# Kernel optimization log

Measured on AMD Instinct MI355X. Metric: run time of the kernel, lower is better.

The kernel has to match this reference:

```python
import jax, jax.numpy as jnp
import numpy as np

B = 4096          # number of instance groups (images)
C = 81            # num_classes + 1 (fixed by the 81x81 prior_rel buffer)
D_K = 64
MAX_N = 128       # max instances per group


def setup_inputs() -> dict:
    key = jax.random.key(0)
    rng = np.random.default_rng(0)
    ni = rng.integers(1, MAX_N + 1, size=B)
    ni[0] = MAX_N  # pin the max so padded length is deterministic
    num_instances = jnp.asarray(ni, dtype=jnp.int32)
    total = int(ni.sum())
    ks = jax.random.split(key, 10)
    s_in = 1.0 / np.sqrt(C)
    s_dk = 1.0 / np.sqrt(D_K)
    return {
        'x': jax.random.normal(ks[0], (total, C), jnp.float32),
        'num_instances': num_instances,
        'prior_rel': jax.random.normal(ks[1], (C, C), jnp.float32) * s_in,
        'wq': jax.random.normal(ks[2], (C, D_K), jnp.float32) * s_in,
        'bq': jnp.zeros((D_K,), jnp.float32),
        'wk': jax.random.normal(ks[3], (C, D_K), jnp.float32) * s_in,
        'bk': jnp.zeros((D_K,), jnp.float32),
        'wv': jax.random.normal(ks[4], (C, D_K), jnp.float32) * s_in,
        'bv': jnp.zeros((D_K,), jnp.float32),
        'wu': jax.random.normal(ks[5], (D_K, C), jnp.float32) * s_dk,
        'bu': jnp.zeros((C,), jnp.float32),
    }


def reference(x, num_instances, prior_rel, wq, bq, wk, bk, wv, bv, wu, bu):
    # num_instances is static ragged metadata (the torch code keeps it as a
    # Python list), so it is safe to pull concrete ints from it here.
    ni = np.asarray(num_instances)
    Bn = ni.shape[0]
    M = int(ni.max())
    total = x.shape[0]

    counts = jnp.asarray(ni, jnp.int32)                      # [B]
    offsets = jnp.concatenate([jnp.zeros((1,), jnp.int32),
                               jnp.cumsum(counts)[:-1]])      # [B]
    pos = jnp.arange(M, dtype=jnp.int32)                      # [M]
    mask = pos[None, :] < counts[:, None]                     # [B, M] valid slots
    idx = offsets[:, None] + pos[None, :]                     # [B, M] flat gather idx
    idx_safe = jnp.where(mask, idx, 0)

    # pad: split x into ragged groups, zero-pad each to length M
    padded = x[idx_safe] * mask[:, :, None].astype(x.dtype)   # [B, M, C]

    q = padded @ wq + bq                                      # [B, M, d_k]
    k = padded @ wk + bk                                      # [B, M, d_k]
    v = (padded @ prior_rel) @ wv + bv                        # [B, M, d_k]

    scores = jnp.einsum('bmd,bnd->bmn', q, k) / jnp.sqrt(
        jnp.asarray(D_K, x.dtype))                            # [B, M, M]
    # mask padded KEY columns (queries on padded rows are dropped at unpad)
    scores = jnp.where(mask[:, None, :], scores, -jnp.inf)
    probs = jax.nn.softmax(scores, axis=2)
    out = jnp.einsum('bmn,bnd->bmd', probs, v)                # [B, M, d_k]
    out = out @ wu + bu                                       # [B, M, C]

    # unpad: scatter valid rows back to their ragged flat positions
    tgt = jnp.where(mask, idx, total)                         # dump pad rows past end
    flat = jnp.zeros((total + 1, out.shape[-1]), out.dtype)
    flat = flat.at[tgt.reshape(-1)].set(out.reshape(-1, out.shape[-1]))
    return flat[:total]
```

## Files before the change

kernel.cpp:

```cpp
#include <hip/hip_runtime.h>


typedef __attribute__((ext_vector_type(8))) short short8;
typedef __attribute__((ext_vector_type(4))) float f32x4;
typedef __attribute__((ext_vector_type(4))) short short4v;

constexpr int C  = 81;
constexpr int DK = 64;
constexpr int CP = 96;

constexpr int QK_STRIDE = 72;
constexpr int VT_STRIDE = 136;
constexpr int P_STRIDE  = 136;
constexpr int QS_STRIDE = 72;
constexpr int O_STRIDE  = 72;
constexpr int OFF_K  = 0;
constexpr int OFF_VT = OFF_K + 128 * QK_STRIDE;
constexpr int OFF_P  = OFF_VT + 64 * VT_STRIDE;
constexpr int SMEM_TOT = OFF_P + 4 * 16 * P_STRIDE;

__device__ inline ushort f2b(float f) {
    uint u = __float_as_uint(f);
    uint r = (u + 0x7fffu + ((u >> 16) & 1u)) >> 16;
    return (ushort)r;
}

#define MFMA16(a, b, c) __builtin_amdgcn_mfma_f32_16x16x32_bf16((a), (b), (c), 0, 0, 0)

__global__ void scan_counts(const int* __restrict__ counts,
                            int* __restrict__ offsets, int n) {
    __shared__ int part[256];
    int tid = threadIdx.x;
    int per = (n + 255) >> 8;
    int base = tid * per;
    int s = 0;
    for (int i = 0; i < per; i++) {
        int idx = base + i;
        if (idx < n) s += counts[idx];
    }
    part[tid] = s;
    __syncthreads();
    for (int off = 1; off < 256; off <<= 1) {
        int v = (tid >= off) ? part[tid - off] : 0;
        __syncthreads();
        part[tid] += v;
        __syncthreads();
    }
    int run = (tid == 0) ? 0 : part[tid - 1];
    for (int i = 0; i < per; i++) {
        int idx = base + i;
        if (idx < n) { offsets[idx] = run; run += counts[idx]; }
    }
}

__global__ void prep_weights(const float* __restrict__ prior,
                             const float* __restrict__ wq, const float* __restrict__ wk,
                             const float* __restrict__ wv, const float* __restrict__ wu,
                             ushort* __restrict__ wqT, ushort* __restrict__ wkT,
                             ushort* __restrict__ wvT, ushort* __restrict__ wuT) {
    int idx = blockIdx.x * 256 + threadIdx.x;
    int sec = idx / (DK * CP);
    int i   = idx - sec * (DK * CP);
    if (sec == 0 || sec == 1) {
        int n = i / CP, k = i - (i / CP) * CP;
        const float* w = (sec == 0) ? wq : wk;
        ushort* dst    = (sec == 0) ? wqT : wkT;
        dst[n * CP + k] = (k < C) ? f2b(w[k * DK + n]) : (ushort)0;
    } else if (sec == 2) {
        int n = i / CP, k = i - (i / CP) * CP;
        float s = 0.f;
        if (k < C)
            for (int e = 0; e < C; e++) s = fmaf(prior[k * C + e], wv[e * DK + n], s);
        wvT[n * CP + k] = (k < C) ? f2b(s) : (ushort)0;
    } else {
        int n = i / DK, k = i - (i / DK) * DK;
        wuT[n * DK + k] = (n < C) ? f2b(wu[k * C + n]) : (ushort)0;
    }
}

__launch_bounds__(256, 3)
__global__ void ravnet_mfma(const float* __restrict__ x,
                            const int* __restrict__ counts,
                            const int* __restrict__ offsets,
                            const ushort* __restrict__ wqT, const ushort* __restrict__ wkT,
                            const ushort* __restrict__ wvT, const ushort* __restrict__ wuT,
                            const float* __restrict__ bq, const float* __restrict__ bk,
                            const float* __restrict__ bv, const float* __restrict__ bu,
                            float* __restrict__ out) {
    __shared__ __align__(16) ushort sm[SMEM_TOT];

    const int b    = blockIdx.x;
    const int N    = counts[b];
    const long off = offsets[b];
    const int tid  = threadIdx.x;
    const int lane = tid & 63;
    const int wave = tid >> 6;
    const int quad = lane >> 4;
    const int m16  = lane & 15;
    const int NT8  = (N + 15) >> 4;
    const int NT4  = (N + 31) >> 5;
    const float* xsrc = x + off * C;

    short4v qreg[2][4];

    #pragma unroll
    for (int t = 0; t < 2; t++) {
        const int rt = wave + 4 * t;
        if (rt < NT8) {
            const int row  = rt * 16 + m16;
            const bool vrow = row < N;
            const float* xr = xsrc + (long)(vrow ? row : (N - 1)) * C;
            short8 ax[3];
            #pragma unroll
            for (int ks = 0; ks < 2; ks++) {
                const int c0 = ks * 32 + quad * 8;
                short8 a;
                #pragma unroll
                for (int e = 0; e < 8; e++) a[e] = (short)f2b(vrow ? xr[c0 + e] : 0.f);
                ax[ks] = a;
            }
            {
                const int c0 = 64 + quad * 8;
                short8 a;
                #pragma unroll
                for (int e = 0; e < 8; e++) {
                    const int c = c0 + e;
                    a[e] = (short)((vrow && c < C) ? f2b(xr[c]) : (ushort)0);
                }
                ax[2] = a;
            }
            #pragma unroll
            for (int nt = 0; nt < 4; nt++) {
                const int n = nt * 16 + m16;
                f32x4 acc = {0.f, 0.f, 0.f, 0.f};
                #pragma unroll
                for (int ks = 0; ks < 3; ks++)
                    acc = MFMA16(ax[ks], *(const short8*)(wqT + n * CP + ks * 32 + quad * 8), acc);
                const float bb = bq[n];
                short4v pk;
                #pragma unroll
                for (int r = 0; r < 4; r++) pk[r] = (short)f2b(acc[r] + bb);
                qreg[t][nt] = pk;
            }
            #pragma unroll
            for (int nt = 0; nt < 4; nt++) {
                const int n = nt * 16 + m16;
                f32x4 acc = {0.f, 0.f, 0.f, 0.f};
                #pragma unroll
                for (int ks = 0; ks < 3; ks++)
                    acc = MFMA16(ax[ks], *(const short8*)(wkT + n * CP + ks * 32 + quad * 8), acc);
                const float bb = bk[n];
                #pragma unroll
                for (int r = 0; r < 4; r++)
                    sm[OFF_K + (rt * 16 + quad * 4 + r) * QK_STRIDE + n] = f2b(acc[r] + bb);
            }
            #pragma unroll
            for (int nt = 0; nt < 4; nt++) {
                const int n = nt * 16 + m16;
                f32x4 acc = {0.f, 0.f, 0.f, 0.f};
                #pragma unroll
                for (int ks = 0; ks < 3; ks++)
                    acc = MFMA16(ax[ks], *(const short8*)(wvT + n * CP + ks * 32 + quad * 8), acc);
                const float bb = bv[n];
                short4v pk;
                #pragma unroll
                for (int r = 0; r < 4; r++) pk[r] = (short)f2b(acc[r] + bb);
                *(short4v*)(sm + OFF_VT + n * VT_STRIDE + rt * 16 + quad * 4) = pk;
            }
        }
    }
    if (NT8 & 1) {
        const int R = NT8 * 16;
        const int d = tid >> 2, c4 = (tid & 3) << 2;
        short4v z = {0, 0, 0, 0};
        *(short4v*)(sm + OFF_VT + d * VT_STRIDE + R + c4) = z;
    }
    __syncthreads();

    ushort* Pw = sm + OFF_P + wave * (16 * P_STRIDE);
    #pragma unroll
    for (int t = 0; t < 2; t++) {
        const int qt = wave + 4 * t;
        if (qt < NT8) {
            #pragma unroll
            for (int nt = 0; nt < 4; nt++) {
                const short4v q4 = qreg[t][nt];
                #pragma unroll
                for (int r = 0; r < 4; r++)
                    Pw[(quad * 4 + r) * QS_STRIDE + nt * 16 + m16] = (ushort)q4[r];
            }
            __threadfence_block();
            short8 aq[2];
            #pragma unroll
            for (int ks = 0; ks < 2; ks++)
                aq[ks] = *(const short8*)(Pw + m16 * QS_STRIDE + ks * 32 + quad * 8);
            f32x4 sacc[8];
            #pragma unroll
            for (int ct = 0; ct < 8; ct++) {
                if (ct < NT8) {
                    f32x4 a = {0.f, 0.f, 0.f, 0.f};
                    #pragma unroll
                    for (int ks = 0; ks < 2; ks++) {
                        short8 kb = *(const short8*)(sm + OFF_K + (ct * 16 + m16) * QK_STRIDE +
                                                     ks * 32 + quad * 8);
                        a = MFMA16(aq[ks], kb, a);
                    }
                    sacc[ct] = a;
                }
            }
            float mr[4] = {-3e38f, -3e38f, -3e38f, -3e38f};
            #pragma unroll
            for (int ct = 0; ct < 8; ct++) if (ct < NT8) {
                const bool valid = (ct * 16 + m16) < N;
                #pragma unroll
                for (int r = 0; r < 4; r++) {
                    float s = valid ? sacc[ct][r] * 0.125f : -3e38f;
                    sacc[ct][r] = s;
                    mr[r] = fmaxf(mr[r], s);
                }
            }
            #pragma unroll
            for (int r = 0; r < 4; r++) {
                mr[r] = fmaxf(mr[r], __shfl_xor(mr[r], 1, 64));
                mr[r] = fmaxf(mr[r], __shfl_xor(mr[r], 2, 64));
                mr[r] = fmaxf(mr[r], __shfl_xor(mr[r], 4, 64));
                mr[r] = fmaxf(mr[r], __shfl_xor(mr[r], 8, 64));
            }
            float lr[4] = {0.f, 0.f, 0.f, 0.f};
            #pragma unroll
            for (int ct = 0; ct < 8; ct++) if (ct < NT8) {
                #pragma unroll
                for (int r = 0; r < 4; r++) {
                    float p = __expf(sacc[ct][r] - mr[r]);
                    sacc[ct][r] = p;
                    lr[r] += p;
                }
            }
            #pragma unroll
            for (int r = 0; r < 4; r++) {
                lr[r] += __shfl_xor(lr[r], 1, 64);
                lr[r] += __shfl_xor(lr[r], 2, 64);
                lr[r] += __shfl_xor(lr[r], 4, 64);
                lr[r] += __shfl_xor(lr[r], 8, 64);
            }
            #pragma unroll
            for (int ct = 0; ct < 8; ct++) if (ct < NT8) {
                #pragma unroll
                for (int r = 0; r < 4; r++)
                    Pw[(quad * 4 + r) * P_STRIDE + ct * 16 + m16] = f2b(sacc[ct][r]);
            }
            if (NT8 & 1) {
                #pragma unroll
                for (int r = 0; r < 4; r++)
                    Pw[(quad * 4 + r) * P_STRIDE + NT8 * 16 + m16] = 0;
            }
            __threadfence_block();
            short8 ap[4];
            #pragma unroll
            for (int kt = 0; kt < 4; kt++) if (kt < NT4)
                ap[kt] = *(const short8*)(Pw + m16 * P_STRIDE + kt * 32 + quad * 8);
            __threadfence_block();
            float linv[4];
            #pragma unroll
            for (int r = 0; r < 4; r++) linv[r] = (lr[r] > 0.f) ? 1.f / lr[r] : 0.f;
            #pragma unroll
            for (int ot = 0; ot < 4; ot++) {
                f32x4 oa = {0.f, 0.f, 0.f, 0.f};
                #pragma unroll
                for (int kt = 0; kt < 4; kt++) if (kt < NT4) {
                    short8 vb = *(const short8*)(sm + OFF_VT + (ot * 16 + m16) * VT_STRIDE +
                                                 kt * 32 + quad * 8);
                    oa = MFMA16(ap[kt], vb, oa);
                }
                #pragma unroll
                for (int r = 0; r < 4; r++)
                    Pw[(quad * 4 + r) * O_STRIDE + ot * 16 + m16] = f2b(oa[r] * linv[r]);
            }
            __threadfence_block();
            short8 ao[2];
            #pragma unroll
            for (int ks = 0; ks < 2; ks++)
                ao[ks] = *(const short8*)(Pw + m16 * O_STRIDE + ks * 32 + quad * 8);
            __threadfence_block();
            #pragma unroll
            for (int ct = 0; ct < 6; ct++) {
                f32x4 acc = {0.f, 0.f, 0.f, 0.f};
                #pragma unroll
                for (int ks = 0; ks < 2; ks++) {
                    short8 wb = *(const short8*)(wuT + (ct * 16 + m16) * DK + ks * 32 + quad * 8);
                    acc = MFMA16(ao[ks], wb, acc);
                }
                const int e = ct * 16 + m16;
                if (e < C) {
                    const float bue = bu[e];
                    #pragma unroll
                    for (int r = 0; r < 4; r++) {
                        const int row = qt * 16 + quad * 4 + r;
                        if (row < N) out[(off + row) * C + e] = acc[r] + bue;
                    }
                }
            }
        }
    }
}

extern "C" void kernel_launch(void* const* d_in, const int* in_sizes, int n_in,
                              void* d_out, int out_size, void* d_ws, size_t ws_size,
                              hipStream_t stream) {
    const float* x      = (const float*)d_in[0];
    const int*   counts = (const int*)  d_in[1];
    const float* prior  = (const float*)d_in[2];
    const float* wq     = (const float*)d_in[3];
    const float* bq     = (const float*)d_in[4];
    const float* wk     = (const float*)d_in[5];
    const float* bk     = (const float*)d_in[6];
    const float* wv     = (const float*)d_in[7];
    const float* bv     = (const float*)d_in[8];
    const float* wu     = (const float*)d_in[9];
    const float* bu     = (const float*)d_in[10];
    float* out = (float*)d_out;

    const int B = in_sizes[1];

    int*    offsets = (int*)d_ws;
    ushort* wqT = (ushort*)((char*)d_ws + (((size_t)B * sizeof(int) + 255) & ~(size_t)255));
    ushort* wkT = wqT + DK * CP;
    ushort* wvT = wkT + DK * CP;
    ushort* wuT = wvT + DK * CP;

    scan_counts<<<1, 256, 0, stream>>>(counts, offsets, B);
    prep_weights<<<(4 * DK * CP + 255) / 256, 256, 0, stream>>>(
        prior, wq, wk, wv, wu, wqT, wkT, wvT, wuT);
    ravnet_mfma<<<B, 256, 0, stream>>>(x, counts, offsets,
                                       wqT, wkT, wvT, wuT,
                                       bq, bk, bv, bu, out);
}
```

Before: 299.3 us.

## Keep attention intermediates in registers via transposed MFMA and lane shuffles

Swaps the MFMA operand order so each lane holds a whole column (one query row), which makes the softmax row reductions cross-quad shuffles instead of 16-lane reductions. Q, P and O are moved into MFMA A-operand layout with lane shuffles rather than a round trip through per-wave shared-memory scratch, and that scratch buffer is removed. The smaller LDS footprint lets the launch bound rise to 4 blocks per CU. Softmax now uses exp2 with a log2e-folded scale. Costs are extra shuffle and select instructions and higher register pressure under the tighter occupancy bound.

Result: faster. 284.5 us (-4.9%).

```diff
diff --git a/kernel.cpp b/kernel.cpp
--- a/kernel.cpp
+++ b/kernel.cpp
@@ -11,19 +11,22 @@
 
 constexpr int QK_STRIDE = 72;
 constexpr int VT_STRIDE = 136;
-constexpr int P_STRIDE  = 136;
-constexpr int QS_STRIDE = 72;
-constexpr int O_STRIDE  = 72;
 constexpr int OFF_K  = 0;
-constexpr int OFF_VT = OFF_K + 128 * QK_STRIDE;
-constexpr int OFF_P  = OFF_VT + 64 * VT_STRIDE;
-constexpr int SMEM_TOT = OFF_P + 4 * 16 * P_STRIDE;
+constexpr int OFF_VT = 128 * QK_STRIDE;
+constexpr int SMEM_TOT = OFF_VT + 64 * VT_STRIDE;
 
 __device__ inline ushort f2b(float f) {
     uint u = __float_as_uint(f);
     uint r = (u + 0x7fffu + ((u >> 16) & 1u)) >> 16;
     return (ushort)r;
 }
+__device__ inline uint pack2bf(float a, float b) {
+    return (uint)f2b(a) | ((uint)f2b(b) << 16);
+}
+__device__ inline uint shflu(uint v, int srcLane) {
+    return (uint)__shfl((int)v, srcLane, 64);
+}
+union U8 { short8 s; uint u[4]; };
 
 #define MFMA16(a, b, c) __builtin_amdgcn_mfma_f32_16x16x32_bf16((a), (b), (c), 0, 0, 0)
 
@@ -78,7 +81,7 @@
     }
 }
 
-__launch_bounds__(256, 3)
+__launch_bounds__(256, 4)
 __global__ void ravnet_mfma(const float* __restrict__ x,
                             const int* __restrict__ counts,
                             const int* __restrict__ offsets,
@@ -101,7 +104,11 @@
     const int NT4  = (N + 31) >> 5;
     const float* xsrc = x + off * C;
 
-    short4v qreg[2][4];
+    const int srcE = ((quad & 1) << 5) + m16;
+    const int srcO = srcE + 16;
+    const bool hi  = (quad >> 1) != 0;
+
+    short8 aq[2][2];
 
     #pragma unroll
     for (int t = 0; t < 2; t++) {
@@ -129,43 +136,55 @@
                 }
                 ax[2] = a;
             }
+            uint qpk[4][2];
             #pragma unroll
             for (int nt = 0; nt < 4; nt++) {
-                const int n = nt * 16 + m16;
                 f32x4 acc = {0.f, 0.f, 0.f, 0.f};
                 #pragma unroll
                 for (int ks = 0; ks < 3; ks++)
-                    acc = MFMA16(ax[ks], *(const short8*)(wqT + n * CP + ks * 32 + quad * 8), acc);
-                const float bb = bq[n];
-                short4v pk;
-                #pragma unroll
-                for (int r = 0; r < 4; r++) pk[r] = (short)f2b(acc[r] + bb);
-                qreg[t][nt] = pk;
+                    acc = MFMA16(*(const short8*)(wqT + (nt * 16 + m16) * CP + ks * 32 + quad * 8),
+                                 ax[ks], acc);
+                const f32x4 b4 = *(const f32x4*)(bq + nt * 16 + quad * 4);
+                qpk[nt][0] = pack2bf(acc[0] + b4[0], acc[1] + b4[1]);
+                qpk[nt][1] = pack2bf(acc[2] + b4[2], acc[3] + b4[3]);
+            }
+            #pragma unroll
+            for (int ks = 0; ks < 2; ks++) {
+                uint a0 = shflu(qpk[2 * ks][0], srcE), b0 = shflu(qpk[2 * ks + 1][0], srcE);
+                uint a1 = shflu(qpk[2 * ks][1], srcE), b1 = shflu(qpk[2 * ks + 1][1], srcE);
+                uint a2 = shflu(qpk[2 * ks][0], srcO), b2 = shflu(qpk[2 * ks + 1][0], srcO);
+                uint a3 = shflu(qpk[2 * ks][1], srcO), b3 = shflu(qpk[2 * ks + 1][1], srcO);
+                U8 u;
+                u.u[0] = hi ? b0 : a0;  u.u[1] = hi ? b1 : a1;
+                u.u[2] = hi ? b2 : a2;  u.u[3] = hi ? b3 : a3;
+                aq[t][ks] = u.s;
             }
             #pragma unroll
             for (int nt = 0; nt < 4; nt++) {
-                const int n = nt * 16 + m16;
                 f32x4 acc = {0.f, 0.f, 0.f, 0.f};
                 #pragma unroll
                 for (int ks = 0; ks < 3; ks++)
-                    acc = MFMA16(ax[ks], *(const short8*)(wkT + n * CP + ks * 32 + quad * 8), acc);
-                const float bb = bk[n];
-                #pragma unroll
-                for (int r = 0; r < 4; r++)
-                    sm[OFF_K + (rt * 16 + quad * 4 + r) * QK_STRIDE + n] = f2b(acc[r] + bb);
+                    acc = MFMA16(*(const short8*)(wkT + (nt * 16 + m16) * CP + ks * 32 + quad * 8),
+                                 ax[ks], acc);
+                const f32x4 b4 = *(const f32x4*)(bk + nt * 16 + quad * 4);
+                short4v pk4;
+                #pragma unroll
+                for (int r = 0; r < 4; r++) pk4[r] = (short)f2b(acc[r] + b4[r]);
+                *(short4v*)(sm + OFF_K + (rt * 16 + m16) * QK_STRIDE + nt * 16 + quad * 4) = pk4;
             }
             #pragma unroll
             for (int nt = 0; nt < 4; nt++) {
-                const int n = nt * 16 + m16;
                 f32x4 acc = {0.f, 0.f, 0.f, 0.f};
                 #pragma unroll
                 for (int ks = 0; ks < 3; ks++)
-                    acc = MFMA16(ax[ks], *(const short8*)(wvT + n * CP + ks * 32 + quad * 8), acc);
-                const float bb = bv[n];
-                short4v pk;
-                #pragma unroll
-                for (int r = 0; r < 4; r++) pk[r] = (short)f2b(acc[r] + bb);
-                *(short4v*)(sm + OFF_VT + n * VT_STRIDE + rt * 16 + quad * 4) = pk;
+                    acc = MFMA16(ax[ks],
+                                 *(const short8*)(wvT + (nt * 16 + m16) * CP + ks * 32 + quad * 8),
+                                 acc);
+                const float bb = bv[nt * 16 + m16];
+                short4v pk4;
+                #pragma unroll
+                for (int r = 0; r < 4; r++) pk4[r] = (short)f2b(acc[r] + bb);
+                *(short4v*)(sm + OFF_VT + (nt * 16 + m16) * VT_STRIDE + rt * 16 + quad * 4) = pk4;
             }
         }
     }
@@ -177,23 +196,11 @@
     }
     __syncthreads();
 
-    ushort* Pw = sm + OFF_P + wave * (16 * P_STRIDE);
+    constexpr float SCALE = 0.18033688011112042f;
     #pragma unroll
     for (int t = 0; t < 2; t++) {
         const int qt = wave + 4 * t;
         if (qt < NT8) {
-            #pragma unroll
-            for (int nt = 0; nt < 4; nt++) {
-                const short4v q4 = qreg[t][nt];
-                #pragma unroll
-                for (int r = 0; r < 4; r++)
-                    Pw[(quad * 4 + r) * QS_STRIDE + nt * 16 + m16] = (ushort)q4[r];
-            }
-            __threadfence_block();
-            short8 aq[2];
-            #pragma unroll
-            for (int ks = 0; ks < 2; ks++)
-                aq[ks] = *(const short8*)(Pw + m16 * QS_STRIDE + ks * 32 + quad * 8);
             f32x4 sacc[8];
             #pragma unroll
             for (int ct = 0; ct < 8; ct++) {
@@ -203,66 +210,62 @@
                     for (int ks = 0; ks < 2; ks++) {
                         short8 kb = *(const short8*)(sm + OFF_K + (ct * 16 + m16) * QK_STRIDE +
                                                      ks * 32 + quad * 8);
-                        a = MFMA16(aq[ks], kb, a);
+                        a = MFMA16(kb, aq[t][ks], a);
                     }
                     sacc[ct] = a;
                 }
             }
-            float mr[4] = {-3e38f, -3e38f, -3e38f, -3e38f};
+            float mr = -3e38f;
             #pragma unroll
             for (int ct = 0; ct < 8; ct++) if (ct < NT8) {
-                const bool valid = (ct * 16 + m16) < N;
                 #pragma unroll
                 for (int r = 0; r < 4; r++) {
-                    float s = valid ? sacc[ct][r] * 0.125f : -3e38f;
+                    const bool valid = (ct * 16 + quad * 4 + r) < N;
+                    float s = valid ? sacc[ct][r] * SCALE : -3e38f;
                     sacc[ct][r] = s;
-                    mr[r] = fmaxf(mr[r], s);
-                }
-            }
-            #pragma unroll
-            for (int r = 0; r < 4; r++) {
-                mr[r] = fmaxf(mr[r], __shfl_xor(mr[r], 1, 64));
-                mr[r] = fmaxf(mr[r], __shfl_xor(mr[r], 2, 64));
-                mr[r] = fmaxf(mr[r], __shfl_xor(mr[r], 4, 64));
-                mr[r] = fmaxf(mr[r], __shfl_xor(mr[r], 8, 64));
-            }
-            float lr[4] = {0.f, 0.f, 0.f, 0.f};
+                    mr = fmaxf(mr, s);
+                }
+            }
+            mr = fmaxf(mr, __shfl_xor(mr, 16, 64));
+            mr = fmaxf(mr, __shfl_xor(mr, 32, 64));
+            float lr = 0.f;
             #pragma unroll
             for (int ct = 0; ct < 8; ct++) if (ct < NT8) {
                 #pragma unroll
                 for (int r = 0; r < 4; r++) {
-                    float p = __expf(sacc[ct][r] - mr[r]);
+                    float p = __builtin_exp2f(sacc[ct][r] - mr);
                     sacc[ct][r] = p;
-                    lr[r] += p;
-                }
-            }
-            #pragma unroll
-            for (int r = 0; r < 4; r++) {
-                lr[r] += __shfl_xor(lr[r], 1, 64);
-                lr[r] += __shfl_xor(lr[r], 2, 64);
-                lr[r] += __shfl_xor(lr[r], 4, 64);
-                lr[r] += __shfl_xor(lr[r], 8, 64);
-            }
-            #pragma unroll
-            for (int ct = 0; ct < 8; ct++) if (ct < NT8) {
-                #pragma unroll
-                for (int r = 0; r < 4; r++)
-                    Pw[(quad * 4 + r) * P_STRIDE + ct * 16 + m16] = f2b(sacc[ct][r]);
-            }
-            if (NT8 & 1) {
-                #pragma unroll
-                for (int r = 0; r < 4; r++)
-                    Pw[(quad * 4 + r) * P_STRIDE + NT8 * 16 + m16] = 0;
-            }
-            __threadfence_block();
+                    lr += p;
+                }
+            }
+            lr += __shfl_xor(lr, 16, 64);
+            lr += __shfl_xor(lr, 32, 64);
+            const float linv = 1.f / lr;
+            uint pk[8][2];
+            #pragma unroll
+            for (int ct = 0; ct < 8; ct++) {
+                if (ct < NT8) {
+                    pk[ct][0] = pack2bf(sacc[ct][0], sacc[ct][1]);
+                    pk[ct][1] = pack2bf(sacc[ct][2], sacc[ct][3]);
+                } else {
+                    pk[ct][0] = 0u; pk[ct][1] = 0u;
+                }
+            }
             short8 ap[4];
             #pragma unroll
-            for (int kt = 0; kt < 4; kt++) if (kt < NT4)
-                ap[kt] = *(const short8*)(Pw + m16 * P_STRIDE + kt * 32 + quad * 8);
-            __threadfence_block();
-            float linv[4];
-            #pragma unroll
-            for (int r = 0; r < 4; r++) linv[r] = (lr[r] > 0.f) ? 1.f / lr[r] : 0.f;
+            for (int kt = 0; kt < 4; kt++) {
+                if (kt < NT4) {
+                    uint a0 = shflu(pk[2 * kt][0], srcE), b0 = shflu(pk[2 * kt + 1][0], srcE);
+                    uint a1 = shflu(pk[2 * kt][1], srcE), b1 = shflu(pk[2 * kt + 1][1], srcE);
+                    uint a2 = shflu(pk[2 * kt][0], srcO), b2 = shflu(pk[2 * kt + 1][0], srcO);
+                    uint a3 = shflu(pk[2 * kt][1], srcO), b3 = shflu(pk[2 * kt + 1][1], srcO);
+                    U8 u;
+                    u.u[0] = hi ? b0 : a0;  u.u[1] = hi ? b1 : a1;
+                    u.u[2] = hi ? b2 : a2;  u.u[3] = hi ? b3 : a3;
+                    ap[kt] = u.s;
+                }
+            }
+            uint opk[4][2];
             #pragma unroll
             for (int ot = 0; ot < 4; ot++) {
                 f32x4 oa = {0.f, 0.f, 0.f, 0.f};
@@ -270,33 +273,37 @@
                 for (int kt = 0; kt < 4; kt++) if (kt < NT4) {
                     short8 vb = *(const short8*)(sm + OFF_VT + (ot * 16 + m16) * VT_STRIDE +
                                                  kt * 32 + quad * 8);
-                    oa = MFMA16(ap[kt], vb, oa);
-                }
-                #pragma unroll
-                for (int r = 0; r < 4; r++)
-                    Pw[(quad * 4 + r) * O_STRIDE + ot * 16 + m16] = f2b(oa[r] * linv[r]);
-            }
-            __threadfence_block();
+                    oa = MFMA16(vb, ap[kt], oa);
+                }
+                opk[ot][0] = pack2bf(oa[0] * linv, oa[1] * linv);
+                opk[ot][1] = pack2bf(oa[2] * linv, oa[3] * linv);
+            }
             short8 ao[2];
             #pragma unroll
-            for (int ks = 0; ks < 2; ks++)
-                ao[ks] = *(const short8*)(Pw + m16 * O_STRIDE + ks * 32 + quad * 8);
-            __threadfence_block();
+            for (int ks = 0; ks < 2; ks++) {
+                uint a0 = shflu(opk[2 * ks][0], srcE), b0 = shflu(opk[2 * ks + 1][0], srcE);
+                uint a1 = shflu(opk[2 * ks][1], srcE), b1 = shflu(opk[2 * ks + 1][1], srcE);
+                uint a2 = shflu(opk[2 * ks][0], srcO), b2 = shflu(opk[2 * ks + 1][0], srcO);
+                uint a3 = shflu(opk[2 * ks][1], srcO), b3 = shflu(opk[2 * ks + 1][1], srcO);
+                U8 u;
+                u.u[0] = hi ? b0 : a0;  u.u[1] = hi ? b1 : a1;
+                u.u[2] = hi ? b2 : a2;  u.u[3] = hi ? b3 : a3;
+                ao[ks] = u.s;
+            }
+            const int row = qt * 16 + m16;
             #pragma unroll
             for (int ct = 0; ct < 6; ct++) {
                 f32x4 acc = {0.f, 0.f, 0.f, 0.f};
                 #pragma unroll
                 for (int ks = 0; ks < 2; ks++) {
                     short8 wb = *(const short8*)(wuT + (ct * 16 + m16) * DK + ks * 32 + quad * 8);
-                    acc = MFMA16(ao[ks], wb, acc);
-                }
-                const int e = ct * 16 + m16;
-                if (e < C) {
-                    const float bue = bu[e];
+                    acc = MFMA16(wb, ao[ks], acc);
+                }
+                if (row < N) {
                     #pragma unroll
                     for (int r = 0; r < 4; r++) {
-                        const int row = qt * 16 + quad * 4 + r;
-                        if (row < N) out[(off + row) * C + e] = acc[r] + bue;
+                        const int e = ct * 16 + quad * 4 + r;
+                        if (e < C) out[(off + row) * C + e] = acc[r] + bu[e];
                     }
                 }
             }
```
